# Optimization experiments

Hardware: AMD Instinct MI355X
Metric: run time of the kernel (lower is better)

Reference implementation:

```python
import jax, jax.numpy as jnp
import numpy as np

AUDIO_DIM, TEXT_DIM, HIDDEN_DIM = 512, 768, 512
B, AUDIO_LEN, TEXT_LEN = 8, 2048, 512


def setup_inputs() -> dict:
    key = jax.random.key(0)
    ks = jax.random.split(key, 9)
    audio_features = jax.random.normal(ks[0], (B, AUDIO_LEN, AUDIO_DIM), dtype=jnp.float32)
    text_features = jax.random.normal(ks[1], (B, TEXT_LEN, TEXT_DIM), dtype=jnp.float32)
    text_mask = jax.random.randint(ks[2], (B, TEXT_LEN), 0, 2).astype(jnp.int32)
    # Linear params (PyTorch default init scale ~ U(-1/sqrt(fan_in), 1/sqrt(fan_in)))
    def lin(kw, kb, fan_in, fan_out):
        bound = 1.0 / np.sqrt(fan_in)
        W = jax.random.uniform(kw, (fan_in, fan_out), minval=-bound, maxval=bound, dtype=jnp.float32)
        b = jax.random.uniform(kb, (fan_out,), minval=-bound, maxval=bound, dtype=jnp.float32)
        return W, b
    Wq, bq = lin(ks[3], ks[4], AUDIO_DIM, HIDDEN_DIM)
    Wk, bk = lin(ks[5], ks[6], TEXT_DIM, HIDDEN_DIM)
    Wv, bv = lin(ks[7], ks[8], TEXT_DIM, HIDDEN_DIM)
    return {
        "audio_features": audio_features,
        "text_features": text_features,
        "Wq": Wq, "bq": bq, "Wk": Wk, "bk": bk, "Wv": Wv, "bv": bv,
        "text_mask": text_mask,
    }


def reference(audio_features, text_features, Wq, bq, Wk, bk, Wv, bv, text_mask):
    scale = HIDDEN_DIM ** -0.5
    q = jnp.einsum("bad,dh->bah", audio_features, Wq) + bq  # (B, A, H)
    k = jnp.einsum("btd,dh->bth", text_features, Wk) + bk   # (B, T, H)
    v = jnp.einsum("btd,dh->bth", text_features, Wv) + bv   # (B, T, H)
    scores = jnp.einsum("bah,bth->bat", q, k) * scale        # (B, A, T)
    mask = text_mask[:, None, :]  # (B, 1, T)
    scores = jnp.where(mask == 0, -jnp.inf, scores)
    attn = jax.nn.softmax(scores, axis=-1)
    # dropout is identity in eval mode
    enhanced_audio = jnp.einsum("bat,bth->bah", attn, v)     # (B, A, H)
    return enhanced_audio
```

## Files before the change

kernel.cpp:

```cpp
#include <hip/hip_runtime.h>
#include <cstdint>
#include <cstddef>

#define AUDIO_DIM 512
#define TEXT_DIM  768
#define HIDDEN    512
#define BATCH     8
#define ALEN      2048
#define TLEN      512

typedef _Float16 half8 __attribute__((ext_vector_type(8)));
typedef _Float16 half4_t __attribute__((ext_vector_type(4)));
typedef float floatx4 __attribute__((ext_vector_type(4)));

#define AS1 __attribute__((address_space(1)))
#define AS3 __attribute__((address_space(3)))

__device__ __forceinline__ void gload_lds16(const void* g, void* l) {
    __builtin_amdgcn_global_load_lds((const AS1 void*)g, (AS3 void*)l, 16, 0, 0);
}

__device__ __forceinline__ int swz(int r) { return (r >> 1) & 3; }

#define VMCNT(N) asm volatile("s_waitcnt vmcnt(" #N ")" ::: "memory")

__global__ __launch_bounds__(256) void prep(
    const float* __restrict__ audio, const float* __restrict__ text,
    const float* __restrict__ Wq, const float* __restrict__ Wk,
    const float* __restrict__ Wv,
    _Float16* __restrict__ audio_h, _Float16* __restrict__ text_h,
    _Float16* __restrict__ Wq_t, _Float16* __restrict__ Wk_t,
    _Float16* __restrict__ Wv_t)
{
    __shared__ _Float16 tt[32 * 33];
    const int bid = blockIdx.x, tid = threadIdx.x;
    if (bid < 11264) {
        const float* src; _Float16* dst; int i;
        if (bid < 8192) { src = audio; dst = audio_h; i = bid * 256 + tid; }
        else            { src = text;  dst = text_h;  i = (bid - 8192) * 256 + tid; }
        float4 v = ((const float4*)src)[i];
        half4_t h;
        h.x = (_Float16)v.x; h.y = (_Float16)v.y; h.z = (_Float16)v.z; h.w = (_Float16)v.w;
        ((half4_t*)dst)[i] = h;
    } else {
        const float* src; _Float16* dst; int R, lb;
        if (bid < 11520)      { lb = bid - 11264; src = Wq; dst = Wq_t; R = 512; }
        else if (bid < 11904) { lb = bid - 11520; src = Wk; dst = Wk_t; R = 768; }
        else                  { lb = bid - 11904; src = Wv; dst = Wv_t; R = 768; }
        const int C = 512;
        const int c0 = (lb & 15) * 32, r0 = (lb >> 4) * 32;
        const int tx = tid & 31, ty = tid >> 5;
#pragma unroll
        for (int i = 0; i < 4; i++) {
            int r = ty + i * 8;
            tt[r * 33 + tx] = (_Float16)src[(size_t)(r0 + r) * C + c0 + tx];
        }
        __syncthreads();
#pragma unroll
        for (int i = 0; i < 4; i++) {
            int r = ty + i * 8;
            dst[(size_t)(c0 + r) * R + r0 + tx] = tt[tx * 33 + r];
        }
    }
}

template <bool OUT16, bool ROWBIAS>
__device__ __forceinline__ void gemm_body(
    const _Float16* __restrict__ A, const _Float16* __restrict__ Bt,
    const float* __restrict__ bias, void* __restrict__ Cp,
    int N, int K, int m0, int n0, _Float16* Asm, _Float16* Bsm)
{
    const int tid = threadIdx.x;
    const int l = tid & 63, w = tid >> 6;
    const int wm = w >> 1, wn = w & 1;
    const int srow = l >> 2, sj = l & 3;
    const int q = l >> 4, c16 = l & 15;

    floatx4 acc[4][4] = {};

    for (int k0 = 0; k0 < K; k0 += 32) {
        if (k0) __syncthreads();
#pragma unroll
        for (int i = 0; i < 2; i++) {
            int rb = (w * 2 + i) * 16;
            int r = rb + srow;
            int cc = sj ^ swz(r);
            gload_lds16(A + (size_t)(m0 + r) * K + k0 + cc * 8, Asm + rb * 32);
            gload_lds16(Bt + (size_t)(n0 + r) * K + k0 + cc * 8, Bsm + rb * 32);
        }
        __syncthreads();

        half8 af[4], bf[4];
#pragma unroll
        for (int t = 0; t < 4; t++) {
            int rA = wm * 64 + t * 16 + c16;
            af[t] = *(const half8*)&Asm[rA * 32 + ((q ^ swz(rA)) << 3)];
            int rB = wn * 64 + t * 16 + c16;
            bf[t] = *(const half8*)&Bsm[rB * 32 + ((q ^ swz(rB)) << 3)];
        }
#pragma unroll
        for (int mi = 0; mi < 4; mi++)
#pragma unroll
            for (int ni = 0; ni < 4; ni++)
                acc[mi][ni] = __builtin_amdgcn_mfma_f32_16x16x32_f16(
                    af[mi], bf[ni], acc[mi][ni], 0, 0, 0);
    }

    if (OUT16) {
        float bcol[4];
        float brow[4][4];
        if (!ROWBIAS) {
#pragma unroll
            for (int ni = 0; ni < 4; ni++)
                bcol[ni] = bias[n0 + wn * 64 + ni * 16 + c16];
        } else {
#pragma unroll
            for (int mi = 0; mi < 4; mi++) {
                float4 b4 = *(const float4*)&bias[m0 + wm * 64 + mi * 16 + q * 4];
                brow[mi][0] = b4.x; brow[mi][1] = b4.y;
                brow[mi][2] = b4.z; brow[mi][3] = b4.w;
            }
        }
        _Float16* C = (_Float16*)Cp;
#pragma unroll
        for (int ni = 0; ni < 4; ni++) {
            int col = n0 + wn * 64 + ni * 16 + c16;
#pragma unroll
            for (int mi = 0; mi < 4; mi++) {
                int row = m0 + wm * 64 + mi * 16 + q * 4;
#pragma unroll
                for (int r = 0; r < 4; r++) {
                    float b = ROWBIAS ? brow[mi][r] : bcol[ni];
                    C[(size_t)(row + r) * N + col] = (_Float16)(acc[mi][ni][r] + b);
                }
            }
        }
    } else {
        float* C = (float*)Cp;
#pragma unroll
        for (int ni = 0; ni < 4; ni++) {
            int col = n0 + wn * 64 + ni * 16 + c16;
#pragma unroll
            for (int mi = 0; mi < 4; mi++) {
                int row = m0 + wm * 64 + mi * 16 + q * 4;
#pragma unroll
                for (int r = 0; r < 4; r++)
                    C[(size_t)(row + r) * N + col] = acc[mi][ni][r];
            }
        }
    }
}

__global__ __launch_bounds__(256, 3) void qkv_gemm(
    const _Float16* __restrict__ audio_h, const _Float16* __restrict__ text_h,
    const _Float16* __restrict__ Wq_t, const _Float16* __restrict__ Wk_t,
    const _Float16* __restrict__ Wv_t,
    const float* __restrict__ bq, const float* __restrict__ bk,
    const float* __restrict__ bv,
    _Float16* __restrict__ Qh, _Float16* __restrict__ Kh,
    _Float16* __restrict__ Vt)
{
    __shared__ __align__(16) _Float16 Asm[128 * 32];
    __shared__ __align__(16) _Float16 Bsm[128 * 32];
    const int bid = blockIdx.x;
    if (bid < 512) {
        int t = (bid & 7) * 64 + (bid >> 3);
        gemm_body<true, false>(audio_h, Wq_t, bq, Qh, 512, 512,
                               (t >> 2) * 128, (t & 3) * 128, Asm, Bsm);
    } else if (bid < 640) {
        int s = bid - 512;
        int t = (s & 7) * 16 + (s >> 3);
        gemm_body<true, false>(text_h, Wk_t, bk, Kh, 512, 768,
                               (t >> 2) * 128, (t & 3) * 128, Asm, Bsm);
    } else {
        int s = bid - 640;
        int t = (s & 7) * 16 + (s >> 3);
        int z = t >> 4, by = (t >> 2) & 3, bx = t & 3;
        gemm_body<true, true>(Wv_t, text_h + (size_t)z * 393216, bv,
                              Vt + (size_t)z * 262144, 512, 768,
                              by * 128, bx * 128, Asm, Bsm);
    }
}


#define STAGE64(SRC, K0, BUF)                                               \
    do {                                                                    \
        _Pragma("unroll")                                                   \
        for (int i_ = 0; i_ < 4; i_++) {                                    \
            int lr_ = i_ * 16 + srow;                                       \
            int cc_ = sj ^ swz(lr_);                                        \
            gload_lds16((SRC) + (size_t)(w * 64 + lr_) * HIDDEN + (K0) + cc_ * 8, \
                        &(BUF)[i_ * 512]);                                  \
        }                                                                   \
    } while (0)

__global__ __launch_bounds__(512, 2) void attn(
    const _Float16* __restrict__ Qh, const _Float16* __restrict__ Kh,
    const _Float16* __restrict__ Vt, const int* __restrict__ mask,
    float* __restrict__ out)
{
    __shared__ __align__(16) _Float16 QPs[64 * 512];
    __shared__ __align__(16) _Float16 Ks[8][2][64 * 32];
    __shared__ float red[8][64];
    __shared__ float red2[8][64];
    const int tid = threadIdx.x, l = tid & 63, w = tid >> 6;
    const int lin = blockIdx.x;
    const int tb = (lin & 7) * 32 + (lin >> 3);
    const int b = tb >> 5, a0 = (tb & 31) * 64;
    const _Float16* Qb = Qh + (size_t)(b * ALEN + a0) * HIDDEN;
    const _Float16* Kb = Kh + (size_t)b * TLEN * HIDDEN;
    const _Float16* Vb = Vt + (size_t)b * TLEN * HIDDEN;
    const int srow = l >> 2, sj = l & 3;
    const int q = l >> 4, c16 = l & 15;

    int mv[4];
#pragma unroll
    for (int ni = 0; ni < 4; ni++)
        mv[ni] = mask[b * TLEN + w * 64 + ni * 16 + c16];

#pragma unroll
    for (int i = 0; i < 8; i++) {
        int r = w * 8 + i;
        gload_lds16(Qb + (size_t)r * 512 + ((l ^ (r & 7)) << 3), &QPs[r * 512]);
    }
    STAGE64(Kb, 0, Ks[w][0]);
    STAGE64(Kb, 32, Ks[w][1]);
    __syncthreads();

    floatx4 acc[4][4] = {};
#pragma unroll
    for (int ks = 0; ks < 16; ks++) {
        const int k0 = ks * 32;
        if (ks == 15) { VMCNT(0); } else { VMCNT(4); }
        half8 af[4], bf[4];
        const _Float16* kb = &Ks[w][ks & 1][0];
#pragma unroll
        for (int t = 0; t < 4; t++) {
            int rA = t * 16 + c16;
            af[t] = *(const half8*)&QPs[rA * 512 + ((((k0 >> 3) + q) ^ (rA & 7)) << 3)];
            bf[t] = *(const half8*)&kb[rA * 32 + ((q ^ swz(rA)) << 3)];
        }
#pragma unroll
        for (int mi = 0; mi < 4; mi++)
#pragma unroll
            for (int ni = 0; ni < 4; ni++)
                acc[mi][ni] = __builtin_amdgcn_mfma_f32_16x16x32_f16(
                    af[mi], bf[ni], acc[mi][ni], 0, 0, 0);
        if (ks < 14) STAGE64(Kb, k0 + 64, Ks[w][ks & 1]);
    }

    STAGE64(Vb, 0, Ks[w][0]);
    STAGE64(Vb, 32, Ks[w][1]);

    const float scale = 0.044194173824159216f;
#pragma unroll
    for (int mi = 0; mi < 4; mi++)
#pragma unroll
        for (int ni = 0; ni < 4; ni++)
#pragma unroll
            for (int r = 0; r < 4; r++)
                acc[mi][ni][r] = mv[ni] ? acc[mi][ni][r] * scale : -1e30f;

    float mx[4][4];
#pragma unroll
    for (int mi = 0; mi < 4; mi++)
#pragma unroll
        for (int r = 0; r < 4; r++) {
            float m = -1e30f;
#pragma unroll
            for (int ni = 0; ni < 4; ni++) m = fmaxf(m, acc[mi][ni][r]);
#pragma unroll
            for (int off = 1; off <= 8; off <<= 1) m = fmaxf(m, __shfl_xor(m, off));
            mx[mi][r] = m;
        }
    if (c16 == 0)
#pragma unroll
        for (int mi = 0; mi < 4; mi++)
#pragma unroll
            for (int r = 0; r < 4; r++) red[w][mi * 16 + q * 4 + r] = mx[mi][r];
    __syncthreads();
#pragma unroll
    for (int mi = 0; mi < 4; mi++)
#pragma unroll
        for (int r = 0; r < 4; r++) {
            int row = mi * 16 + q * 4 + r;
            float m = red[0][row];
#pragma unroll
            for (int ww = 1; ww < 8; ww++) m = fmaxf(m, red[ww][row]);
            mx[mi][r] = m;
        }

    float sm[4][4];
#pragma unroll
    for (int mi = 0; mi < 4; mi++)
#pragma unroll
        for (int r = 0; r < 4; r++) {
            float s = 0.f;
#pragma unroll
            for (int ni = 0; ni < 4; ni++) {
                float e = __expf(acc[mi][ni][r] - mx[mi][r]);
                acc[mi][ni][r] = e;
                s += e;
            }
#pragma unroll
            for (int off = 1; off <= 8; off <<= 1) s += __shfl_xor(s, off);
            sm[mi][r] = s;
        }
    if (c16 == 0)
#pragma unroll
        for (int mi = 0; mi < 4; mi++)
#pragma unroll
            for (int r = 0; r < 4; r++) red2[w][mi * 16 + q * 4 + r] = sm[mi][r];
    __syncthreads();

    _Float16* Ps = QPs;
#pragma unroll
    for (int mi = 0; mi < 4; mi++)
#pragma unroll
        for (int r = 0; r < 4; r++) {
            int row = mi * 16 + q * 4 + r;
            float s = red2[0][row];
#pragma unroll
            for (int ww = 1; ww < 8; ww++) s += red2[ww][row];
            float inv = 1.f / s;
#pragma unroll
            for (int ni = 0; ni < 4; ni++) {
                int col = w * 64 + ni * 16 + c16;
                Ps[row * 512 + ((((col >> 3) ^ (row & 7)) << 3) + (col & 7))] =
                    (_Float16)(acc[mi][ni][r] * inv);
            }
        }
    __syncthreads();

    floatx4 oacc[4][4] = {};
#pragma unroll
    for (int ts = 0; ts < 16; ts++) {
        const int t0 = ts * 32;
        if (ts == 15) { VMCNT(0); } else { VMCNT(4); }
        half8 af[4], bf[4];
        const _Float16* vb = &Ks[w][ts & 1][0];
#pragma unroll
        for (int t = 0; t < 4; t++) {
            int rA = t * 16 + c16;
            af[t] = *(const half8*)&Ps[rA * 512 + ((((t0 >> 3) + q) ^ (rA & 7)) << 3)];
            bf[t] = *(const half8*)&vb[rA * 32 + ((q ^ swz(rA)) << 3)];
        }
#pragma unroll
        for (int mi = 0; mi < 4; mi++)
#pragma unroll
            for (int ni = 0; ni < 4; ni++)
                oacc[mi][ni] = __builtin_amdgcn_mfma_f32_16x16x32_f16(
                    af[mi], bf[ni], oacc[mi][ni], 0, 0, 0);
        if (ts < 14) STAGE64(Vb, t0 + 64, Ks[w][ts & 1]);
    }

    float* Ob = out + (size_t)(b * ALEN + a0) * HIDDEN;
#pragma unroll
    for (int ni = 0; ni < 4; ni++) {
        int col = w * 64 + ni * 16 + c16;
#pragma unroll
        for (int mi = 0; mi < 4; mi++) {
            int row = mi * 16 + q * 4;
#pragma unroll
            for (int r = 0; r < 4; r++)
                Ob[(size_t)(row + r) * HIDDEN + col] = oacc[mi][ni][r];
        }
    }
}

extern "C" void kernel_launch(void* const* d_in, const int* in_sizes, int n_in,
                              void* d_out, int out_size, void* d_ws, size_t ws_size,
                              hipStream_t stream)
{
    const float* audio = (const float*)d_in[0];
    const float* text  = (const float*)d_in[1];
    const float* Wq    = (const float*)d_in[2];
    const float* bq    = (const float*)d_in[3];
    const float* Wk    = (const float*)d_in[4];
    const float* bk    = (const float*)d_in[5];
    const float* Wv    = (const float*)d_in[6];
    const float* bv    = (const float*)d_in[7];
    const int*   maskp = (const int*)d_in[8];
    float* out = (float*)d_out;

    _Float16* audio_h = (_Float16*)d_out;
    _Float16* Qh      = audio_h + (size_t)8388608;

    _Float16* ws16   = (_Float16*)d_ws;
    _Float16* text_h = ws16;
    _Float16* Wq_t   = text_h + 3145728;
    _Float16* Wk_t   = Wq_t + 262144;
    _Float16* Wv_t   = Wk_t + 393216;
    _Float16* Kh     = Wv_t + 393216;
    _Float16* Vt     = Kh + 2097152;

    prep<<<12288, 256, 0, stream>>>(audio, text, Wq, Wk, Wv,
                                    audio_h, text_h, Wq_t, Wk_t, Wv_t);
    qkv_gemm<<<768, 256, 0, stream>>>(audio_h, text_h, Wq_t, Wk_t, Wv_t,
                                      bq, bk, bv, Qh, Kh, Vt);
    attn<<<256, 512, 0, stream>>>(Qh, Kh, Vt, maskp, out);
}
```

Measured before the change: 165.2 us.

## Fuse audio fp16 conversion into Q GEMM and reorder attention loop staging

The separate fp32-to-fp16 pass over the audio tensor is removed; the Q projection GEMM now loads fp32 audio directly and converts it while writing LDS, saving a full write and re-read of a 16 MB intermediate. In the attention kernel, Q/P fragment reads are issued before waiting on the K/V staging loads. The next tile's global-to-LDS prefetch is issued right after LDS reads complete rather than after the MFMAs. MFMA blocks also get raised wave priority. The trade-off is that the Q GEMM's A operand now goes through registers with synchronous fp32 loads instead of async LDS loads, which may expose latency.

```diff
diff --git a/kernel.cpp b/kernel.cpp
--- a/kernel.cpp
+++ b/kernel.cpp
@@ -23,30 +23,33 @@
 __device__ __forceinline__ int swz(int r) { return (r >> 1) & 3; }
 
 #define VMCNT(N) asm volatile("s_waitcnt vmcnt(" #N ")" ::: "memory")
+#define LDS_READS_DONE()                                    \
+    do {                                                    \
+        asm volatile("s_waitcnt lgkmcnt(0)" ::: "memory");  \
+        __builtin_amdgcn_sched_barrier(0);                  \
+    } while (0)
 
 __global__ __launch_bounds__(256) void prep(
-    const float* __restrict__ audio, const float* __restrict__ text,
+    const float* __restrict__ text,
     const float* __restrict__ Wq, const float* __restrict__ Wk,
     const float* __restrict__ Wv,
-    _Float16* __restrict__ audio_h, _Float16* __restrict__ text_h,
+    _Float16* __restrict__ text_h,
     _Float16* __restrict__ Wq_t, _Float16* __restrict__ Wk_t,
     _Float16* __restrict__ Wv_t)
 {
     __shared__ _Float16 tt[32 * 33];
     const int bid = blockIdx.x, tid = threadIdx.x;
-    if (bid < 11264) {
-        const float* src; _Float16* dst; int i;
-        if (bid < 8192) { src = audio; dst = audio_h; i = bid * 256 + tid; }
-        else            { src = text;  dst = text_h;  i = (bid - 8192) * 256 + tid; }
-        float4 v = ((const float4*)src)[i];
+    if (bid < 3072) {
+        int i = bid * 256 + tid;
+        float4 v = ((const float4*)text)[i];
         half4_t h;
         h.x = (_Float16)v.x; h.y = (_Float16)v.y; h.z = (_Float16)v.z; h.w = (_Float16)v.w;
-        ((half4_t*)dst)[i] = h;
+        ((half4_t*)text_h)[i] = h;
     } else {
         const float* src; _Float16* dst; int R, lb;
-        if (bid < 11520)      { lb = bid - 11264; src = Wq; dst = Wq_t; R = 512; }
-        else if (bid < 11904) { lb = bid - 11520; src = Wk; dst = Wk_t; R = 768; }
-        else                  { lb = bid - 11904; src = Wv; dst = Wv_t; R = 768; }
+        if (bid < 3328)      { lb = bid - 3072; src = Wq; dst = Wq_t; R = 512; }
+        else if (bid < 3712) { lb = bid - 3328; src = Wk; dst = Wk_t; R = 768; }
+        else                 { lb = bid - 3712; src = Wv; dst = Wv_t; R = 768; }
         const int C = 512;
         const int c0 = (lb & 15) * 32, r0 = (lb >> 4) * 32;
         const int tx = tid & 31, ty = tid >> 5;
@@ -64,9 +67,9 @@
     }
 }
 
-template <bool OUT16, bool ROWBIAS>
+template <bool OUT16, bool ROWBIAS, bool CVT_A>
 __device__ __forceinline__ void gemm_body(
-    const _Float16* __restrict__ A, const _Float16* __restrict__ Bt,
+    const void* __restrict__ Avp, const _Float16* __restrict__ Bt,
     const float* __restrict__ bias, void* __restrict__ Cp,
     int N, int K, int m0, int n0, _Float16* Asm, _Float16* Bsm)
 {
@@ -85,7 +88,21 @@
             int rb = (w * 2 + i) * 16;
             int r = rb + srow;
             int cc = sj ^ swz(r);
-            gload_lds16(A + (size_t)(m0 + r) * K + k0 + cc * 8, Asm + rb * 32);
+            if constexpr (CVT_A) {
+                const float* Af = (const float*)Avp;
+                const float* s = &Af[(size_t)(m0 + r) * K + k0 + cc * 8];
+                float4 v0 = *(const float4*)s;
+                float4 v1 = *(const float4*)(s + 4);
+                half8 h;
+                h[0] = (_Float16)v0.x; h[1] = (_Float16)v0.y;
+                h[2] = (_Float16)v0.z; h[3] = (_Float16)v0.w;
+                h[4] = (_Float16)v1.x; h[5] = (_Float16)v1.y;
+                h[6] = (_Float16)v1.z; h[7] = (_Float16)v1.w;
+                *(half8*)&Asm[r * 32 + sj * 8] = h;
+            } else {
+                const _Float16* Ah = (const _Float16*)Avp;
+                gload_lds16(Ah + (size_t)(m0 + r) * K + k0 + cc * 8, Asm + rb * 32);
+            }
             gload_lds16(Bt + (size_t)(n0 + r) * K + k0 + cc * 8, Bsm + rb * 32);
         }
         __syncthreads();
@@ -152,7 +169,7 @@
 }
 
 __global__ __launch_bounds__(256, 3) void qkv_gemm(
-    const _Float16* __restrict__ audio_h, const _Float16* __restrict__ text_h,
+    const float* __restrict__ audio, const _Float16* __restrict__ text_h,
     const _Float16* __restrict__ Wq_t, const _Float16* __restrict__ Wk_t,
     const _Float16* __restrict__ Wv_t,
     const float* __restrict__ bq, const float* __restrict__ bk,
@@ -165,23 +182,22 @@
     const int bid = blockIdx.x;
     if (bid < 512) {
         int t = (bid & 7) * 64 + (bid >> 3);
-        gemm_body<true, false>(audio_h, Wq_t, bq, Qh, 512, 512,
-                               (t >> 2) * 128, (t & 3) * 128, Asm, Bsm);
+        gemm_body<true, false, true>(audio, Wq_t, bq, Qh, 512, 512,
+                                     (t >> 2) * 128, (t & 3) * 128, Asm, Bsm);
     } else if (bid < 640) {
         int s = bid - 512;
         int t = (s & 7) * 16 + (s >> 3);
-        gemm_body<true, false>(text_h, Wk_t, bk, Kh, 512, 768,
-                               (t >> 2) * 128, (t & 3) * 128, Asm, Bsm);
+        gemm_body<true, false, false>(text_h, Wk_t, bk, Kh, 512, 768,
+                                      (t >> 2) * 128, (t & 3) * 128, Asm, Bsm);
     } else {
         int s = bid - 640;
         int t = (s & 7) * 16 + (s >> 3);
         int z = t >> 4, by = (t >> 2) & 3, bx = t & 3;
-        gemm_body<true, true>(Wv_t, text_h + (size_t)z * 393216, bv,
-                              Vt + (size_t)z * 262144, 512, 768,
-                              by * 128, bx * 128, Asm, Bsm);
-    }
-}
-
+        gemm_body<true, true, false>(Wv_t, text_h + (size_t)z * 393216, bv,
+                                     Vt + (size_t)z * 262144, 512, 768,
+                                     by * 128, bx * 128, Asm, Bsm);
+    }
+}
 
 #define STAGE64(SRC, K0, BUF)                                               \
     do {                                                                    \
@@ -231,22 +247,29 @@
 #pragma unroll
     for (int ks = 0; ks < 16; ks++) {
         const int k0 = ks * 32;
-        if (ks == 15) { VMCNT(0); } else { VMCNT(4); }
         half8 af[4], bf[4];
-        const _Float16* kb = &Ks[w][ks & 1][0];
 #pragma unroll
         for (int t = 0; t < 4; t++) {
             int rA = t * 16 + c16;
             af[t] = *(const half8*)&QPs[rA * 512 + ((((k0 >> 3) + q) ^ (rA & 7)) << 3)];
+        }
+        if (ks == 15) { VMCNT(0); } else { VMCNT(4); }
+        const _Float16* kb = &Ks[w][ks & 1][0];
+#pragma unroll
+        for (int t = 0; t < 4; t++) {
+            int rA = t * 16 + c16;
             bf[t] = *(const half8*)&kb[rA * 32 + ((q ^ swz(rA)) << 3)];
         }
+        LDS_READS_DONE();
+        if (ks < 14) STAGE64(Kb, k0 + 64, Ks[w][ks & 1]);
+        __builtin_amdgcn_s_setprio(1);
 #pragma unroll
         for (int mi = 0; mi < 4; mi++)
 #pragma unroll
             for (int ni = 0; ni < 4; ni++)
                 acc[mi][ni] = __builtin_amdgcn_mfma_f32_16x16x32_f16(
                     af[mi], bf[ni], acc[mi][ni], 0, 0, 0);
-        if (ks < 14) STAGE64(Kb, k0 + 64, Ks[w][ks & 1]);
+        __builtin_amdgcn_s_setprio(0);
     }
 
     STAGE64(Vb, 0, Ks[w][0]);
@@ -336,22 +359,29 @@
 #pragma unroll
     for (int ts = 0; ts < 16; ts++) {
         const int t0 = ts * 32;
-        if (ts == 15) { VMCNT(0); } else { VMCNT(4); }
         half8 af[4], bf[4];
-        const _Float16* vb = &Ks[w][ts & 1][0];
 #pragma unroll
         for (int t = 0; t < 4; t++) {
             int rA = t * 16 + c16;
             af[t] = *(const half8*)&Ps[rA * 512 + ((((t0 >> 3) + q) ^ (rA & 7)) << 3)];
+        }
+        if (ts == 15) { VMCNT(0); } else { VMCNT(4); }
+        const _Float16* vb = &Ks[w][ts & 1][0];
+#pragma unroll
+        for (int t = 0; t < 4; t++) {
+            int rA = t * 16 + c16;
             bf[t] = *(const half8*)&vb[rA * 32 + ((q ^ swz(rA)) << 3)];
         }
+        LDS_READS_DONE();
+        if (ts < 14) STAGE64(Vb, t0 + 64, Ks[w][ts & 1]);
+        __builtin_amdgcn_s_setprio(1);
 #pragma unroll
         for (int mi = 0; mi < 4; mi++)
 #pragma unroll
             for (int ni = 0; ni < 4; ni++)
                 oacc[mi][ni] = __builtin_amdgcn_mfma_f32_16x16x32_f16(
                     af[mi], bf[ni], oacc[mi][ni], 0, 0, 0);
-        if (ts < 14) STAGE64(Vb, t0 + 64, Ks[w][ts & 1]);
+        __builtin_amdgcn_s_setprio(0);
     }
 
     float* Ob = out + (size_t)(b * ALEN + a0) * HIDDEN;
@@ -383,8 +413,7 @@
     const int*   maskp = (const int*)d_in[8];
     float* out = (float*)d_out;
 
-    _Float16* audio_h = (_Float16*)d_out;
-    _Float16* Qh      = audio_h + (size_t)8388608;
+    _Float16* Qh = (_Float16*)d_out + (size_t)8388608;
 
     _Float16* ws16   = (_Float16*)d_ws;
     _Float16* text_h = ws16;
@@ -394,9 +423,9 @@
     _Float16* Kh     = Wv_t + 393216;
     _Float16* Vt     = Kh + 2097152;
 
-    prep<<<12288, 256, 0, stream>>>(audio, text, Wq, Wk, Wv,
-                                    audio_h, text_h, Wq_t, Wk_t, Wv_t);
-    qkv_gemm<<<768, 256, 0, stream>>>(audio_h, text_h, Wq_t, Wk_t, Wv_t,
+    prep<<<4096, 256, 0, stream>>>(text, Wq, Wk, Wv,
+                                   text_h, Wq_t, Wk_t, Wv_t);
+    qkv_gemm<<<768, 256, 0, stream>>>(audio, text_h, Wq_t, Wk_t, Wv_t,
                                       bq, bk, bv, Qh, Kh, Vt);
     attn<<<256, 512, 0, stream>>>(Qh, Kh, Vt, maskp, out);
 }
```

Result: slower. 170.5 us (+3.2%).
